# Kernel optimization log

Hardware: AMD Instinct MI355X
Metric: run time of the kernel (lower is better)

The kernel has to match this reference:

```python
import jax, jax.numpy as jnp
import numpy as np

B, A, OBS, HID, MSG, NH, NACT = 4096, 32, 128, 256, 64, 4, 16


def _mha(x, Wqkv, bqkv, Wo, bo, h):
    # torch nn.MultiheadAttention self-attention, batch_first
    b, a, m = x.shape
    qkv = x @ Wqkv.T + bqkv                      # [B,A,3M]
    q, k, v = jnp.split(qkv, 3, axis=-1)
    dh = m // h
    sh = lambda t: t.reshape(b, a, h, dh).transpose(0, 2, 1, 3)  # [B,H,A,dh]
    q, k, v = sh(q), sh(k), sh(v)
    att = jax.nn.softmax(jnp.einsum('bhqd,bhkd->bhqk', q, k) / jnp.sqrt(jnp.float32(dh)), axis=-1)
    o = jnp.einsum('bhqk,bhkd->bhqd', att, v).transpose(0, 2, 1, 3).reshape(b, a, m)
    return o @ Wo.T + bo


def setup_inputs() -> dict:
    key = jax.random.key(0)
    ks = jax.random.split(key, 24)
    p = lambda i, shape, s=0.05: (jax.random.normal(ks[i], shape, dtype=jnp.float32) * s)
    return {
        'obs': jax.random.normal(ks[0], (B, A, OBS), dtype=jnp.float32),
        'eps_intra': jax.random.normal(ks[1], (B, A, MSG), dtype=jnp.float32),
        'eps_inter': jax.random.normal(ks[2], (B, A, MSG), dtype=jnp.float32),
        'W_local': p(3, (HID, OBS)), 'b_local': p(4, (HID,)),
        'W_inter': p(5, (MSG, OBS)), 'b_inter': p(6, (MSG,)),
        'W_intra': p(7, (MSG, OBS)), 'b_intra': p(8, (MSG,)),
        # 4 attention nets: [intra_mu, intra_std, inter_mu, inter_std]
        'Wqkv': p(9, (4, 3 * MSG, MSG)), 'bqkv': p(10, (4, 3 * MSG)),
        'Wo': p(11, (4, MSG, MSG)), 'bo': p(12, (4, MSG)),
        'att_w': p(13, (1, MSG)), 'att_b': p(14, (1,)),
        'W1': p(15, (HID, HID + 2 * MSG)), 'b1': p(16, (HID,)),
        'W2': p(17, (HID, HID)), 'b2': p(18, (HID,)),
        'Wa': p(19, (NACT, HID)), 'ba': p(20, (NACT,)),
        'Wv': p(21, (1, HID)), 'bv': p(22, (1,)),
        'att_head': NH,
    }


def reference(obs, eps_intra, eps_inter, W_local, b_local, W_inter, b_inter,
              W_intra, b_intra, Wqkv, bqkv, Wo, bo, att_w, att_b,
              W1, b1, W2, b2, Wa, ba, Wv, bv, att_head):
    # embeddings
    local = jnp.tanh(obs @ W_local.T + b_local)            # [B,A,HID]
    inter_e = jnp.tanh(obs @ W_inter.T + b_inter)          # [B,A,MSG]
    intra_e = jnp.tanh(obs @ W_intra.T + b_intra)          # [B,A,MSG]
    # intra_com: mu/std attention + reparameterise
    intra_mu = _mha(intra_e, Wqkv[0], bqkv[0], Wo[0], bo[0], att_head)
    intra_std = jax.nn.softplus(_mha(intra_e, Wqkv[1], bqkv[1], Wo[1], bo[1], att_head) - 5.0)
    intra_obs = intra_mu + intra_std * eps_intra
    # inter_com
    inter_mu = _mha(inter_e, Wqkv[2], bqkv[2], Wo[2], bo[2], att_head)
    inter_std = jax.nn.softplus(_mha(inter_e, Wqkv[3], bqkv[3], Wo[3], bo[3], att_head) - 5.0)
    inter_obs = inter_mu + inter_std * eps_inter
    # pooling over agents (dim=0 in per-env code == axis=1 with batch dim)
    score = jax.nn.softmax(inter_obs @ att_w.T + att_b, axis=1)   # [B,A,1]
    pooled = jnp.sum(score * inter_obs, axis=1, keepdims=True)    # [B,1,MSG]
    pooled_b = jnp.broadcast_to(pooled, inter_obs.shape)
    # AgentAC.forward
    final_obs = jnp.concatenate([local, intra_obs, pooled_b], axis=-1)
    h = jnp.tanh(final_obs @ W1.T + b1)
    h = jnp.tanh(h @ W2.T + b2)
    a = jax.nn.log_softmax(h @ Wa.T + ba, axis=-1)
    v = h @ Wv.T + bv
    return (a, v)
```

## Files before the change

### kernel.cpp

```cpp
#include <hip/hip_runtime.h>

#define BB 4096
#define AA_ 32
#define OBSD 128
#define HIDD 256
#define MSGD 64
#define NHH 4
#define DHH 16
#define NACTD 16
#define NT 512

#define OFF_WLOCAL 0
#define OFF_WINTER 32768
#define OFF_WINTRA 40960
#define OFF_WQKV   49152
#define OFF_WO     98304
#define OFF_W1     114688
#define OFF_W2     212992
#define OFF_WA     278528
#define OFF_WHEAD  282624
#define WS_TOTAL   290816

#define L_LB 0
#define L_IE 16896
#define L_NE 21504
#define L_IO 26112
#define L_QK 30720
#define L_VT 39424
#define L_AT 44544
#define L_SC 49152
#define SMEM_SZ 49664

typedef unsigned short u16;
typedef unsigned int u32;
typedef __attribute__((ext_vector_type(8))) short bf16x8;
typedef __attribute__((ext_vector_type(4))) float f32x4;

#define MFMA16(a, b, c) __builtin_amdgcn_mfma_f32_16x16x32_bf16((a), (b), (c), 0, 0, 0)

__device__ __forceinline__ float b2f(u16 s) { return __uint_as_float((u32)s << 16); }
__device__ __forceinline__ u16 f2b(float f) {
    u32 u = __float_as_uint(f);
    u += 0x7FFFu + ((u >> 16) & 1u);
    return (u16)(u >> 16);
}
__device__ __forceinline__ float tof(float x) { return x; }
// ... 22 lines not shown
    } else {
        const float* p = (const float*)Wf + (size_t)n * ldw + k;
        f32x4 f0 = *(const f32x4*)(p);
        f32x4 f1 = *(const f32x4*)(p + 4);
#pragma unroll
        for (int j = 0; j < 8; j++) {
            float fv = (j < 4) ? f0[j] : f1[j - 4];
            u16 h = f2b(fv);
            bh[j] = (short)h;
            bl[j] = (short)f2b(fv - b2f(h));
        }
    }
}

template<int N, int K, int ACT, int WM, typename T>
__device__ __forceinline__ void mdense(const u16* X, int ldx,
                                       const T* Wf, const u16* Whi, const u16* Wlo,
                                       const T* bias, u16* O, int ldo) {
    const int tid = threadIdx.x;
    const int wv = tid >> 6, lo16 = tid & 15, hi = (tid & 63) >> 4;
#pragma unroll 1
    for (int nt = wv; nt < N / 16; nt += 8) {
        f32x4 acc0 = {0.f, 0.f, 0.f, 0.f}, acc1 = {0.f, 0.f, 0.f, 0.f};
#pragma unroll
        for (int k0 = 0; k0 < K; k0 += 32) {
            bf16x8 bh, bl;
            loadW<WM>(Wf, Whi, Wlo, K, nt * 16 + lo16, k0 + hi * 8, bh, bl);
            bf16x8 a0 = *(const bf16x8*)(X + lo16 * ldx + k0 + hi * 8);
            bf16x8 a1 = *(const bf16x8*)(X + (16 + lo16) * ldx + k0 + hi * 8);
            acc0 = MFMA16(a0, bh, acc0);
            acc1 = MFMA16(a1, bh, acc1);
            if constexpr (WM == 1) {
                acc0 = MFMA16(a0, bl, acc0);
                acc1 = MFMA16(a1, bl, acc1);
            }
        }
        float bb = tof(bias[nt * 16 + lo16]);
#pragma unroll
        for (int r = 0; r < 4; r++) {
            float v0 = acc0[r] + bb, v1 = acc1[r] + bb;
            if (ACT) { v0 = fast_tanh(v0); v1 = fast_tanh(v1); }
            O[(hi * 4 + r) * ldo + nt * 16 + lo16] = f2b(v0);
            O[(16 + hi * 4 + r) * ldo + nt * 16 + lo16] = f2b(v1);
        }
    }
}

template<int WM, typename T>
__device__ __forceinline__ void qkv_pass(int net, const u16* xe,
                                         const T* Wqkv, const T* bqkv,
                                         const u16* wsh, const u16* wsl,
                                         u16* qk, u16* vT) {
    const int tid = threadIdx.x;
    const int wv = tid >> 6, lo16 = tid & 15, hi = (tid & 63) >> 4;
    const T* Wq = Wqkv + (size_t)net * 192 * MSGD;
    const T* bq_ = bqkv + (size_t)net * 192;
    const u16* Whi = (WM == 2) ? wsh + OFF_WQKV + net * 192 * MSGD : nullptr;
    const u16* Wlo = (WM == 2) ? wsl + OFF_WQKV + net * 192 * MSGD : nullptr;
#pragma unroll 1
    for (int nt = wv; nt < 12; nt += 8) {
        f32x4 acc0 = {0.f, 0.f, 0.f, 0.f}, acc1 = {0.f, 0.f, 0.f, 0.f};
#pragma unroll
        for (int k0 = 0; k0 < 64; k0 += 32) {
            bf16x8 bh, bl;
            loadW<WM>(Wq, Whi, Wlo, 64, nt * 16 + lo16, k0 + hi * 8, bh, bl);
            bf16x8 a0 = *(const bf16x8*)(xe + lo16 * 72 + k0 + hi * 8);
            bf16x8 a1 = *(const bf16x8*)(xe + (16 + lo16) * 72 + k0 + hi * 8);
            acc0 = MFMA16(a0, bh, acc0);
            acc1 = MFMA16(a1, bh, acc1);
            if constexpr (WM == 1) {
                acc0 = MFMA16(a0, bl, acc0);
                acc1 = MFMA16(a1, bl, acc1);
            }
        }
        float bb = tof(bq_[nt * 16 + lo16]);
        if (nt < 8) {
#pragma unroll
            for (int r = 0; r < 4; r++) {
                qk[(hi * 4 + r) * 136 + nt * 16 + lo16] = f2b(acc0[r] + bb);
                qk[(16 + hi * 4 + r) * 136 + nt * 16 + lo16] = f2b(acc1[r] + bb);
            }
        } else {
            const int d = (nt - 8) * 16 + lo16;
#pragma unroll
            for (int r = 0; r < 4; r++) {
                vT[d * 40 + hi * 4 + r] = f2b(acc0[r] + bb);
                vT[d * 40 + 16 + hi * 4 + r] = f2b(acc1[r] + bb);
            }
        }
    }
}

template<typename T, int WM>
__device__ void body(const T* obs, const T* eps_intra, const T* eps_inter,
                     const T* W_local, const T* b_local,
                     const T* W_inter, const T* b_inter,
                     const T* W_intra, const T* b_intra,
                     const T* Wqkv, const T* bqkv, const T* Wo, const T* bo,
                     const T* att_w, const T* att_b,
                     const T* W1, const T* b1, const T* W2, const T* b2,
                     const T* Wa, const T* ba, const T* Wv, const T* bv,
                     T* out_a, T* out_v, char* smem, const u16* wsw) {
    constexpr bool XSPLIT = (sizeof(T) == 4) && (WM == 1);
    const int tid = threadIdx.x;
    const int b = blockIdx.x;
    const int wv = tid >> 6, lane = tid & 63, lo16 = lane & 15, hi = lane >> 4;

    const u16* wsh = wsw;
    const u16* wsl = (WM == 2) ? wsw + WS_TOTAL : nullptr;
#define WPAIR(OFF) ((WM == 2) ? wsh + (OFF) : nullptr), ((WM == 2) ? wsl + (OFF) : nullptr)

    u16* localb    = (u16*)(smem + L_LB);
    u16* intra_e   = (u16*)(smem + L_IE);
    u16* nobs      = (u16*)(smem + L_IE);
    float* alog    = (float*)(smem + L_IE);
    u16* inter_e   = (u16*)(smem + L_NE);
    u16* iobs      = (u16*)(smem + L_IO);
    u16* qk        = (u16*)(smem + L_QK);
    u16* xh        = (u16*)(smem + L_QK);
    u16* hb        = (u16*)(smem + L_QK);
    u16* vT        = (u16*)(smem + L_VT);
    u16* xl        = (u16*)(smem + L_VT);
    u16* atto      = (u16*)(smem + L_AT);
    u16* pooled_hi = (u16*)(smem + L_SC);
    u16* pooled_lo = (u16*)(smem + L_SC + 128);
    float* plog    = (float*)(smem + L_SC + 256);
    float* pscore  = (float*)(smem + L_SC + 384);

    {
        const T* ob = obs + (size_t)b * (AA_ * OBSD);
        const int i = tid;
        const int row = i >> 4, col = (i & 15) * 8;
        if constexpr (sizeof(T) == 4) {
            f32x4 f0 = __builtin_nontemporal_load((const f32x4*)(ob + i * 8));
            f32x4 f1 = __builtin_nontemporal_load((const f32x4*)(ob + i * 8) + 1);
            bf16x8 vh, vl;
#pragma unroll
            for (int j = 0; j < 8; j++) {
                float fv = (j < 4) ? f0[j] : f1[j - 4];
                u16 h = f2b(fv);
                vh[j] = (short)h;
                vl[j] = (short)f2b(fv - b2f(h));
            }
            *(bf16x8*)(xh + row * 136 + col) = vh;
            if constexpr (XSPLIT) *(bf16x8*)(xl + row * 136 + col) = vl;
        } else {
            bf16x8 v = __builtin_nontemporal_load((const bf16x8*)(ob + i * 8));
            *(bf16x8*)(xh + row * 136 + col) = v;
        }
        if (tid < 32) *(bf16x8*)(xh + tid * 136 + 128) = bzero8();
    }
    __syncthreads();

#pragma unroll 1
    for (int u = wv; u < 24; u += 8) {
        const T *Wf, *bias; const u16 *Whi = nullptr, *Wlo = nullptr; u16* O; int ldo, nt;
        if (u < 16)      { Wf = W_local; bias = b_local; O = localb;  ldo = 264; nt = u;
                           if (WM == 2) { Whi = wsh + OFF_WLOCAL; Wlo = wsl + OFF_WLOCAL; } }
        else if (u < 20) { Wf = W_intra; bias = b_intra; O = intra_e; ldo = 72;  nt = u - 16;
                           if (WM == 2) { Whi = wsh + OFF_WINTRA; Wlo = wsl + OFF_WINTRA; } }
        else             { Wf = W_inter; bias = b_inter; O = inter_e; ldo = 72;  nt = u - 20;
                           if (WM == 2) { Whi = wsh + OFF_WINTER; Wlo = wsl + OFF_WINTER; } }
        f32x4 acc0 = {0.f, 0.f, 0.f, 0.f}, acc1 = {0.f, 0.f, 0.f, 0.f};
#pragma unroll
        for (int k0 = 0; k0 < OBSD; k0 += 32) {
            bf16x8 bh, bl;
            loadW<WM>(Wf, Whi, Wlo, OBSD, nt * 16 + lo16, k0 + hi * 8, bh, bl);
            bf16x8 a0 = *(const bf16x8*)(xh + lo16 * 136 + k0 + hi * 8);
            bf16x8 a1 = *(const bf16x8*)(xh + (16 + lo16) * 136 + k0 + hi * 8);
            acc0 = MFMA16(a0, bh, acc0);
            acc1 = MFMA16(a1, bh, acc1);
            if constexpr (WM == 1) {
                acc0 = MFMA16(a0, bl, acc0);
                acc1 = MFMA16(a1, bl, acc1);
            }
            if constexpr (XSPLIT) {
                bf16x8 l0 = *(const bf16x8*)(xl + lo16 * 136 + k0 + hi * 8);
                bf16x8 l1 = *(const bf16x8*)(xl + (16 + lo16) * 136 + k0 + hi * 8);
                acc0 = MFMA16(l0, bh, acc0);
                acc1 = MFMA16(l1, bh, acc1);
            }
        }
        float bb = tof(bias[nt * 16 + lo16]);
#pragma unroll
        for (int r = 0; r < 4; r++) {
            O[(hi * 4 + r) * ldo + nt * 16 + lo16] = f2b(fast_tanh(acc0[r] + bb));
            O[(16 + hi * 4 + r) * ldo + nt * 16 + lo16] = f2b(fast_tanh(acc1[r] + bb));
        }
    }
    __syncthreads();

#pragma unroll 1
    for (int net = 0; net < 4; net++) {
        qkv_pass<WM>(net, (net < 2) ? intra_e : inter_e, Wqkv, bqkv, wsh, wsl, qk, vT);
        __syncthreads();

        float epr[4] = {0.f, 0.f, 0.f, 0.f};
        {
            const int h = wv >> 1, mt = wv & 1;
            if (net == 1 || net == 3) {
                const T* epsb = ((net == 1) ? eps_intra : eps_inter) + (size_t)b * (AA_ * MSGD);
                const int ntU = wv & 3, half = wv >> 2, col = ntU * 16 + lo16;
#pragma unroll
                for (int r = 0; r < 4; r++)
                    epr[r] = tof(__builtin_nontemporal_load(epsb + (half * 16 + hi * 4 + r) * MSGD + col));
            }
            bf16x8 a0 = *(const bf16x8*)(qk + lo16 * 136 + 64 + h * 16 + hi * 8);
            bf16x8 a1 = *(const bf16x8*)(qk + (16 + lo16) * 136 + 64 + h * 16 + hi * 8);
            bf16x8 bq = bzero8();
            if (hi < 2) bq = *(const bf16x8*)(qk + (mt * 16 + lo16) * 136 + h * 16 + hi * 8);
            f32x4 z = {0.f, 0.f, 0.f, 0.f};
            f32x4 sc0 = MFMA16(a0, bq, z);
            f32x4 sc1 = MFMA16(a1, bq, z);
            float v0[4], v1[4];
#pragma unroll
            for (int r = 0; r < 4; r++) { v0[r] = sc0[r] * 0.25f; v1[r] = sc1[r] * 0.25f; }
            float m = fmaxf(fmaxf(fmaxf(v0[0], v0[1]), fmaxf(v0[2], v0[3])),
                            fmaxf(fmaxf(v1[0], v1[1]), fmaxf(v1[2], v1[3])));
            m = fmaxf(m, __shfl_xor(m, 16));
            m = fmaxf(m, __shfl_xor(m, 32));
            float e0[4], e1[4], s = 0.f;
#pragma unroll
            for (int r = 0; r < 4; r++) {
                e0[r] = __expf(v0[r] - m); e1[r] = __expf(v1[r] - m);
                s += e0[r] + e1[r];
            }
            s += __shfl_xor(s, 16);
            s += __shfl_xor(s, 32);
            float inv = __builtin_amdgcn_rcpf(s);
            u32 pk0 = (u32)f2b(e0[0] * inv) | ((u32)f2b(e0[1] * inv) << 16);
            u32 pk1 = (u32)f2b(e0[2] * inv) | ((u32)f2b(e0[3] * inv) << 16);
            u32 pk2 = (u32)f2b(e1[0] * inv) | ((u32)f2b(e1[1] * inv) << 16);
            u32 pk3 = (u32)f2b(e1[2] * inv) | ((u32)f2b(e1[3] * inv) << 16);
            const int sA = (((hi * 2) & 3) << 4) | lo16;
            const int sB = sA + 16;
            u32 wA0 = __shfl(pk0, sA), wA1 = __shfl(pk1, sA);
            u32 wB0 = __shfl(pk0, sB), wB1 = __shfl(pk1, sB);
            u32 xA0 = __shfl(pk2, sA), xA1 = __shfl(pk3, sA);
            u32 xB0 = __shfl(pk2, sB), xB1 = __shfl(pk3, sB);
            const bool lo = (hi < 2);
            union { u32 w[4]; bf16x8 v; } pu;
            pu.w[0] = lo ? wA0 : xA0;
            pu.w[1] = lo ? wA1 : xA1;
            pu.w[2] = lo ? wB0 : xB0;
            pu.w[3] = lo ? wB1 : xB1;
            bf16x8 bv_ = *(const bf16x8*)(vT + (h * 16 + lo16) * 40 + hi * 8);
            f32x4 o = MFMA16(pu.v, bv_, z);
#pragma unroll
            for (int r = 0; r < 4; r++)
                atto[(mt * 16 + hi * 4 + r) * 72 + h * 16 + lo16] = f2b(o[r]);
        }
        __syncthreads();

        {
            const T* Won = Wo + (size_t)net * MSGD * MSGD;
            const T* bon = bo + (size_t)net * MSGD;
            const u16* Ohi = (WM == 2) ? wsh + OFF_WO + net * 4096 : nullptr;
            const u16* Olo = (WM == 2) ? wsl + OFF_WO + net * 4096 : nullptr;
            const int ntU = wv & 3, half = wv >> 2, col = ntU * 16 + lo16;
            f32x4 acc = {0.f, 0.f, 0.f, 0.f};
#pragma unroll
            for (int k0 = 0; k0 < 64; k0 += 32) {
                bf16x8 bh, bl;
                loadW<WM>(Won, Ohi, Olo, 64, col, k0 + hi * 8, bh, bl);
                bf16x8 a = *(const bf16x8*)(atto + (half * 16 + lo16) * 72 + k0 + hi * 8);
                acc = MFMA16(a, bh, acc);
                if constexpr (WM == 1) acc = MFMA16(a, bl, acc);
            }
            float bb = tof(bon[col]);
            u16* tgt = (net < 2) ? iobs : nobs;
#pragma unroll
            for (int r = 0; r < 4; r++) {
                const int row = half * 16 + hi * 4 + r;
                if (net == 0 || net == 2) {
                    tgt[row * 72 + col] = f2b(acc[r] + bb);
                } else {
                    float zv = acc[r] + bb - 5.f;
                    float sp = (zv > 20.f) ? zv : __logf(1.f + __expf(zv));
                    tgt[row * 72 + col] = f2b(b2f(tgt[row * 72 + col]) + sp * epr[r]);
                }
            }
        }
        __syncthreads();
    }

    if (tid < 64) {
        if (tid < 32) {
            float acc = tof(att_b[0]);
            const u16* xr = nobs + tid * 72;
#pragma unroll
            for (int j = 0; j < 64; j += 8) {
                bf16x8 x = *(const bf16x8*)(xr + j);
#pragma unroll
                for (int jj = 0; jj < 8; jj++) acc = fmaf(b2f((u16)x[jj]), tof(att_w[j + jj]), acc);
            }
            plog[tid] = acc;
        }
        __builtin_amdgcn_wave_barrier();
        if (tid < 32) {
            float m = -1e30f;
            for (int a2 = 0; a2 < 32; a2++) m = fmaxf(m, plog[a2]);
            float s = 0.f;
            for (int a2 = 0; a2 < 32; a2++) s += __expf(plog[a2] - m);
            pscore[tid] = __expf(plog[tid] - m) * __builtin_amdgcn_rcpf(s);
        }
        __builtin_amdgcn_wave_barrier();
        {
            float p = 0.f;
            for (int a2 = 0; a2 < 32; a2++) p = fmaf(pscore[a2], b2f(nobs[a2 * 72 + tid]), p);
            u16 h = f2b(p);
            pooled_hi[tid] = h;
            pooled_lo[tid] = f2b(p - b2f(h));
        }
    }
    __syncthreads();

#pragma unroll 1
    for (int nt = wv; nt < 16; nt += 8) {
        const int n = nt * 16 + lo16;
        f32x4 acc0 = {0.f, 0.f, 0.f, 0.f}, acc1 = {0.f, 0.f, 0.f, 0.f};
        f32x4 accp = {0.f, 0.f, 0.f, 0.f};
#pragma unroll
        for (int k0 = 0; k0 < 256; k0 += 32) {
            bf16x8 bh, bl;
            loadW<WM>(W1, WPAIR(OFF_W1), 384, n, k0 + hi * 8, bh, bl);
            bf16x8 a0 = *(const bf16x8*)(localb + lo16 * 264 + k0 + hi * 8);
            bf16x8 a1 = *(const bf16x8*)(localb + (16 + lo16) * 264 + k0 + hi * 8);
            acc0 = MFMA16(a0, bh, acc0);
            acc1 = MFMA16(a1, bh, acc1);
            if constexpr (WM == 1) { acc0 = MFMA16(a0, bl, acc0); acc1 = MFMA16(a1, bl, acc1); }
        }
#pragma unroll
        for (int k0 = 0; k0 < 64; k0 += 32) {
            bf16x8 bh, bl;
            loadW<WM>(W1, WPAIR(OFF_W1), 384, n, 256 + k0 + hi * 8, bh, bl);
            bf16x8 a0 = *(const bf16x8*)(iobs + lo16 * 72 + k0 + hi * 8);
            bf16x8 a1 = *(const bf16x8*)(iobs + (16 + lo16) * 72 + k0 + hi * 8);
            acc0 = MFMA16(a0, bh, acc0);
            acc1 = MFMA16(a1, bh, acc1);
            if constexpr (WM == 1) { acc0 = MFMA16(a0, bl, acc0); acc1 = MFMA16(a1, bl, acc1); }
        }
#pragma unroll
        for (int k0 = 0; k0 < 64; k0 += 32) {
            bf16x8 bh, bl;
            loadW<WM>(W1, WPAIR(OFF_W1), 384, n, 320 + k0 + hi * 8, bh, bl);
            bf16x8 pa  = *(const bf16x8*)(pooled_hi + k0 + hi * 8);
            bf16x8 pal = *(const bf16x8*)(pooled_lo + k0 + hi * 8);
            accp = MFMA16(pa, bh, accp);
            accp = MFMA16(pal, bh, accp);
            if constexpr (WM == 1) accp = MFMA16(pa, bl, accp);
        }
        float bb = tof(b1[n]) + accp[0];
#pragma unroll
        for (int r = 0; r < 4; r++) {
            hb[(hi * 4 + r) * 264 + n] = f2b(fast_tanh(acc0[r] + bb));
            hb[(16 + hi * 4 + r) * 264 + n] = f2b(fast_tanh(acc1[r] + bb));
        }
    }
    __syncthreads();

    mdense<256, 256, 1, WM>(hb, 264, W2, WPAIR(OFF_W2), b2, localb, 264);
    __syncthreads();

    if constexpr (WM == 2) {
        if (wv < 4) {
            const int ntU = wv & 1, half = wv >> 1;
            const u16* Hhi = wsh + OFF_WHEAD;
            f32x4 acc = {0.f, 0.f, 0.f, 0.f};
#pragma unroll
            for (int k0 = 0; k0 < 256; k0 += 32) {
                bf16x8 bh = *(const bf16x8*)(Hhi + (size_t)(ntU * 16 + lo16) * 256 + k0 + hi * 8);
                bf16x8 a = *(const bf16x8*)(localb + (half * 16 + lo16) * 264 + k0 + hi * 8);
                acc = MFMA16(a, bh, acc);
            }
#pragma unroll
            for (int r = 0; r < 4; r++) {
                const int row = half * 16 + hi * 4 + r;
                if (ntU == 0) alog[row * 18 + lo16] = acc[r] + tof(ba[lo16]);
                else if (lo16 == 0) out_v[(size_t)b * 32 + row] = fromf<T>(acc[r] + tof(bv[0]));
            }
        }
    } else {
        if (wv == 0) {
            f32x4 acc0 = {0.f, 0.f, 0.f, 0.f}, acc1 = {0.f, 0.f, 0.f, 0.f};
#pragma unroll
            for (int k0 = 0; k0 < 256; k0 += 32) {
                bf16x8 bh, bl;
                loadW<WM>(Wa, nullptr, nullptr, 256, lo16, k0 + hi * 8, bh, bl);
                bf16x8 a0 = *(const bf16x8*)(localb + lo16 * 264 + k0 + hi * 8);
                bf16x8 a1 = *(const bf16x8*)(localb + (16 + lo16) * 264 + k0 + hi * 8);
                acc0 = MFMA16(a0, bh, acc0);
                acc1 = MFMA16(a1, bh, acc1);
                if constexpr (WM == 1) { acc0 = MFMA16(a0, bl, acc0); acc1 = MFMA16(a1, bl, acc1); }
            }
            float bb = tof(ba[lo16]);
#pragma unroll
            for (int r = 0; r < 4; r++) {
                alog[(hi * 4 + r) * 18 + lo16] = acc0[r] + bb;
                alog[(16 + hi * 4 + r) * 18 + lo16] = acc1[r] + bb;
            }
        } else if (wv == 1 && lane < 32) {
            const u16* xr = localb + lane * 264;
            float acc = tof(bv[0]);
            for (int k0 = 0; k0 < 256; k0 += 8) {
                bf16x8 x = *(const bf16x8*)(xr + k0);
#pragma unroll
                for (int j = 0; j < 8; j++) acc = fmaf(b2f((u16)x[j]), tof(Wv[k0 + j]), acc);
            }
            out_v[(size_t)b * 32 + lane] = fromf<T>(acc);
        }
    }
    __syncthreads();
    if (tid < 32) {
        const float* lr = alog + tid * 18;
        float m = -1e30f;
#pragma unroll
        for (int n = 0; n < 16; n++) m = fmaxf(m, lr[n]);
        float s = 0.f;
#pragma unroll
        for (int n = 0; n < 16; n++) s += __expf(lr[n] - m);
        float lse = m + __logf(s);
        if constexpr (sizeof(T) == 2) {
            bf16x8 o0, o1;
#pragma unroll
            for (int n = 0; n < 8; n++) {
                o0[n] = (short)f2b(lr[n] - lse);
                o1[n] = (short)f2b(lr[8 + n] - lse);
            }
            bf16x8* oa = (bf16x8*)((u16*)out_a + ((size_t)b * 32 + tid) * 16);
            oa[0] = o0; oa[1] = o1;
        } else {
            float* oa = (float*)out_a + ((size_t)b * 32 + tid) * 16;
#pragma unroll
            for (int g = 0; g < 4; g++) {
                f32x4 t = {lr[4 * g] - lse, lr[4 * g + 1] - lse,
                           lr[4 * g + 2] - lse, lr[4 * g + 3] - lse};
                *(f32x4*)(oa + 4 * g) = t;
            }
        }
    }
#undef WPAIR
}

__device__ __forceinline__ int detect_f32(const void* obs) {
    const unsigned short* u = (const unsigned short*)obs;
    int e = ((int)u[threadIdx.x & 63] >> 7) & 0xFF;
    return __ballot(e >= 0x90) != 0ull;
// ... 16 lines not shown
        if (i < OFF_WINTER)      { src = (const float*)Wl;  off = OFF_WLOCAL; }
        else if (i < OFF_WINTRA) { src = (const float*)Wi;  off = OFF_WINTER; }
        else if (i < OFF_WQKV)   { src = (const float*)Wt;  off = OFF_WINTRA; }
        else if (i < OFF_WO)     { src = (const float*)Wq;  off = OFF_WQKV; }
        else if (i < OFF_W1)     { src = (const float*)Wo_; off = OFF_WO; }
        else if (i < OFF_W2)     { src = (const float*)W1_; off = OFF_W1; }
        else if (i < OFF_WA)     { src = (const float*)W2_; off = OFF_W2; }
        else                     { src = (const float*)Wa_; off = OFF_WA; }
        w = src[i - off];
    }
    u16 h = f2b(w);
    ws[i] = h;
    ws[WS_TOTAL + i] = f2b(w - b2f(h));
}

extern "C" __global__ void __launch_bounds__(NT, 6)
TeamCommAgent_53077205844655_kernel(
    const void* obs, const void* eps_intra, const void* eps_inter,
    const void* W_local, const void* b_local,
    const void* W_inter, const void* b_inter,
    const void* W_intra, const void* b_intra,
    const void* Wqkv, const void* bqkv, const void* Wo, const void* bo,
    const void* att_w, const void* att_b,
    const void* W1, const void* b1, const void* W2, const void* b2,
    const void* Wa, const void* ba, const void* Wv, const void* bv,
    void* out, const u16* wsw) {
    __shared__ __align__(16) char smem[SMEM_SZ];
    if (detect_f32(obs)) {
        if (wsw) {
            body<float, 2>((const float*)obs, (const float*)eps_intra, (const float*)eps_inter,
                           (const float*)W_local, (const float*)b_local,
// ... 35 lines not shown
                     (const u16*)Wv, (const u16*)bv,
                     (u16*)out, (u16*)out + (size_t)BB * AA_ * NACTD, smem, nullptr);
    }
}

extern "C" void kernel_launch(void* const* d_in, const int* in_sizes, int n_in,
                              void* d_out, int out_size, void* d_ws, size_t ws_size,
                              hipStream_t stream) {
    const bool use_ws = (d_ws != nullptr) &&
                        (ws_size >= (size_t)(2 * WS_TOTAL) * sizeof(u16));
    if (use_ws) {
        TeamCommAgent_prep_kernel<<<dim3((WS_TOTAL + 255) / 256), dim3(256), 0, stream>>>(
            d_in[0], d_in[3], d_in[5], d_in[7], d_in[9], d_in[11],
            d_in[15], d_in[17], d_in[19], d_in[21], (u16*)d_ws);
    }
    TeamCommAgent_53077205844655_kernel<<<dim3(BB), dim3(NT), 0, stream>>>(
        d_in[0], d_in[1], d_in[2], d_in[3], d_in[4], d_in[5], d_in[6],
        d_in[7], d_in[8], d_in[9], d_in[10], d_in[11], d_in[12], d_in[13],
        d_in[14], d_in[15], d_in[16], d_in[17], d_in[18], d_in[19], d_in[20],
        d_in[21], d_in[22], d_out, use_ws ? (const u16*)d_ws : nullptr);
}
```

Measured before the change: 477.4 us.

## Process two batch elements per block to reuse weight loads across 64 rows

Result: no change. 480.8 us (+0.7%).

```diff
diff --git a/kernel.cpp b/kernel.cpp
--- a/kernel.cpp
+++ b/kernel.cpp
@@ -22,14 +22,14 @@
 #define WS_TOTAL   290816
 
 #define L_LB 0
-#define L_IE 16896
-#define L_NE 21504
-#define L_IO 26112
-#define L_QK 30720
-#define L_VT 39424
-#define L_AT 44544
-#define L_SC 49152
-#define SMEM_SZ 49664
+#define L_IO 33792
+#define L_IE 43008
+#define L_NE 52224
+#define L_QK 61440
+#define L_VT 78848
+#define L_AT 89088
+#define L_SC 98304
+#define SMEM_SZ 99328
 
 typedef unsigned short u16;
 typedef unsigned int u32;
@@ -82,34 +82,43 @@
 }
 
 template<int N, int K, int ACT, int WM, typename T>
-__device__ __forceinline__ void mdense(const u16* X, int ldx,
-                                       const T* Wf, const u16* Whi, const u16* Wlo,
-                                       const T* bias, u16* O, int ldo) {
+__device__ __forceinline__ void mdense64(const u16* X, int ldx,
+                                         const T* Wf, const u16* Whi, const u16* Wlo,
+                                         const T* bias, u16* O, int ldo) {
     const int tid = threadIdx.x;
     const int wv = tid >> 6, lo16 = tid & 15, hi = (tid & 63) >> 4;
 #pragma unroll 1
     for (int nt = wv; nt < N / 16; nt += 8) {
-        f32x4 acc0 = {0.f, 0.f, 0.f, 0.f}, acc1 = {0.f, 0.f, 0.f, 0.f};
+        f32x4 acc0 = {0.f,0.f,0.f,0.f}, acc1 = {0.f,0.f,0.f,0.f};
+        f32x4 acc2 = {0.f,0.f,0.f,0.f}, acc3 = {0.f,0.f,0.f,0.f};
 #pragma unroll
         for (int k0 = 0; k0 < K; k0 += 32) {
             bf16x8 bh, bl;
             loadW<WM>(Wf, Whi, Wlo, K, nt * 16 + lo16, k0 + hi * 8, bh, bl);
             bf16x8 a0 = *(const bf16x8*)(X + lo16 * ldx + k0 + hi * 8);
             bf16x8 a1 = *(const bf16x8*)(X + (16 + lo16) * ldx + k0 + hi * 8);
+            bf16x8 a2 = *(const bf16x8*)(X + (32 + lo16) * ldx + k0 + hi * 8);
+            bf16x8 a3 = *(const bf16x8*)(X + (48 + lo16) * ldx + k0 + hi * 8);
             acc0 = MFMA16(a0, bh, acc0);
             acc1 = MFMA16(a1, bh, acc1);
+            acc2 = MFMA16(a2, bh, acc2);
+            acc3 = MFMA16(a3, bh, acc3);
             if constexpr (WM == 1) {
                 acc0 = MFMA16(a0, bl, acc0);
                 acc1 = MFMA16(a1, bl, acc1);
+                acc2 = MFMA16(a2, bl, acc2);
+                acc3 = MFMA16(a3, bl, acc3);
             }
         }
         float bb = tof(bias[nt * 16 + lo16]);
 #pragma unroll
         for (int r = 0; r < 4; r++) {
-            float v0 = acc0[r] + bb, v1 = acc1[r] + bb;
-            if (ACT) { v0 = fast_tanh(v0); v1 = fast_tanh(v1); }
+            float v0 = acc0[r] + bb, v1 = acc1[r] + bb, v2 = acc2[r] + bb, v3 = acc3[r] + bb;
+            if (ACT) { v0 = fast_tanh(v0); v1 = fast_tanh(v1); v2 = fast_tanh(v2); v3 = fast_tanh(v3); }
             O[(hi * 4 + r) * ldo + nt * 16 + lo16] = f2b(v0);
             O[(16 + hi * 4 + r) * ldo + nt * 16 + lo16] = f2b(v1);
+            O[(32 + hi * 4 + r) * ldo + nt * 16 + lo16] = f2b(v2);
+            O[(48 + hi * 4 + r) * ldo + nt * 16 + lo16] = f2b(v3);
         }
     }
 }
@@ -127,18 +136,25 @@
     const u16* Wlo = (WM == 2) ? wsl + OFF_WQKV + net * 192 * MSGD : nullptr;
 #pragma unroll 1
     for (int nt = wv; nt < 12; nt += 8) {
-        f32x4 acc0 = {0.f, 0.f, 0.f, 0.f}, acc1 = {0.f, 0.f, 0.f, 0.f};
+        f32x4 acc0 = {0.f,0.f,0.f,0.f}, acc1 = {0.f,0.f,0.f,0.f};
+        f32x4 acc2 = {0.f,0.f,0.f,0.f}, acc3 = {0.f,0.f,0.f,0.f};
 #pragma unroll
         for (int k0 = 0; k0 < 64; k0 += 32) {
             bf16x8 bh, bl;
             loadW<WM>(Wq, Whi, Wlo, 64, nt * 16 + lo16, k0 + hi * 8, bh, bl);
             bf16x8 a0 = *(const bf16x8*)(xe + lo16 * 72 + k0 + hi * 8);
             bf16x8 a1 = *(const bf16x8*)(xe + (16 + lo16) * 72 + k0 + hi * 8);
+            bf16x8 a2 = *(const bf16x8*)(xe + (32 + lo16) * 72 + k0 + hi * 8);
+            bf16x8 a3 = *(const bf16x8*)(xe + (48 + lo16) * 72 + k0 + hi * 8);
             acc0 = MFMA16(a0, bh, acc0);
             acc1 = MFMA16(a1, bh, acc1);
+            acc2 = MFMA16(a2, bh, acc2);
+            acc3 = MFMA16(a3, bh, acc3);
             if constexpr (WM == 1) {
                 acc0 = MFMA16(a0, bl, acc0);
                 acc1 = MFMA16(a1, bl, acc1);
+                acc2 = MFMA16(a2, bl, acc2);
+                acc3 = MFMA16(a3, bl, acc3);
             }
         }
         float bb = tof(bq_[nt * 16 + lo16]);
@@ -147,6 +163,8 @@
             for (int r = 0; r < 4; r++) {
                 qk[(hi * 4 + r) * 136 + nt * 16 + lo16] = f2b(acc0[r] + bb);
                 qk[(16 + hi * 4 + r) * 136 + nt * 16 + lo16] = f2b(acc1[r] + bb);
+                qk[(32 + hi * 4 + r) * 136 + nt * 16 + lo16] = f2b(acc2[r] + bb);
+                qk[(48 + hi * 4 + r) * 136 + nt * 16 + lo16] = f2b(acc3[r] + bb);
             }
         } else {
             const int d = (nt - 8) * 16 + lo16;
@@ -154,6 +172,8 @@
             for (int r = 0; r < 4; r++) {
                 vT[d * 40 + hi * 4 + r] = f2b(acc0[r] + bb);
                 vT[d * 40 + 16 + hi * 4 + r] = f2b(acc1[r] + bb);
+                vT[2560 + d * 40 + hi * 4 + r] = f2b(acc2[r] + bb);
+                vT[2560 + d * 40 + 16 + hi * 4 + r] = f2b(acc3[r] + bb);
             }
         }
     }
@@ -171,7 +191,7 @@
                      T* out_a, T* out_v, char* smem, const u16* wsw) {
     constexpr bool XSPLIT = (sizeof(T) == 4) && (WM == 1);
     const int tid = threadIdx.x;
-    const int b = blockIdx.x;
+    const size_t b0 = (size_t)blockIdx.x * 2;
     const int wv = tid >> 6, lane = tid & 63, lo16 = lane & 15, hi = lane >> 4;
 
     const u16* wsh = wsw;
@@ -179,44 +199,47 @@
 #define WPAIR(OFF) ((WM == 2) ? wsh + (OFF) : nullptr), ((WM == 2) ? wsl + (OFF) : nullptr)
 
     u16* localb    = (u16*)(smem + L_LB);
+    u16* iobs      = (u16*)(smem + L_IO);
+    float* alog    = (float*)(smem + L_IO);
     u16* intra_e   = (u16*)(smem + L_IE);
     u16* nobs      = (u16*)(smem + L_IE);
-    float* alog    = (float*)(smem + L_IE);
+    u16* hb        = (u16*)(smem + L_IE);
     u16* inter_e   = (u16*)(smem + L_NE);
-    u16* iobs      = (u16*)(smem + L_IO);
     u16* qk        = (u16*)(smem + L_QK);
     u16* xh        = (u16*)(smem + L_QK);
-    u16* hb        = (u16*)(smem + L_QK);
     u16* vT        = (u16*)(smem + L_VT);
     u16* xl        = (u16*)(smem + L_VT);
     u16* atto      = (u16*)(smem + L_AT);
     u16* pooled_hi = (u16*)(smem + L_SC);
-    u16* pooled_lo = (u16*)(smem + L_SC + 128);
-    float* plog    = (float*)(smem + L_SC + 256);
-    float* pscore  = (float*)(smem + L_SC + 384);
+    u16* pooled_lo = (u16*)(smem + L_SC + 256);
+    float* plog    = (float*)(smem + L_SC + 512);
+    float* pscore  = (float*)(smem + L_SC + 768);
 
     {
-        const T* ob = obs + (size_t)b * (AA_ * OBSD);
-        const int i = tid;
-        const int row = i >> 4, col = (i & 15) * 8;
-        if constexpr (sizeof(T) == 4) {
-            f32x4 f0 = __builtin_nontemporal_load((const f32x4*)(ob + i * 8));
-            f32x4 f1 = __builtin_nontemporal_load((const f32x4*)(ob + i * 8) + 1);
-            bf16x8 vh, vl;
-#pragma unroll
-            for (int j = 0; j < 8; j++) {
-                float fv = (j < 4) ? f0[j] : f1[j - 4];
-                u16 h = f2b(fv);
-                vh[j] = (short)h;
-                vl[j] = (short)f2b(fv - b2f(h));
-            }
-            *(bf16x8*)(xh + row * 136 + col) = vh;
-            if constexpr (XSPLIT) *(bf16x8*)(xl + row * 136 + col) = vl;
-        } else {
-            bf16x8 v = __builtin_nontemporal_load((const bf16x8*)(ob + i * 8));
-            *(bf16x8*)(xh + row * 136 + col) = v;
-        }
-        if (tid < 32) *(bf16x8*)(xh + tid * 136 + 128) = bzero8();
+        const T* ob = obs + b0 * (AA_ * OBSD);
+#pragma unroll
+        for (int it = 0; it < 2; it++) {
+            const int i = tid + it * NT;
+            const int row = i >> 4, col = (i & 15) * 8;
+            if constexpr (sizeof(T) == 4) {
+                f32x4 f0 = __builtin_nontemporal_load((const f32x4*)(ob + i * 8));
+                f32x4 f1 = __builtin_nontemporal_load((const f32x4*)(ob + i * 8) + 1);
+                bf16x8 vh, vl;
+#pragma unroll
+                for (int j = 0; j < 8; j++) {
+                    float fv = (j < 4) ? f0[j] : f1[j - 4];
+                    u16 h = f2b(fv);
+                    vh[j] = (short)h;
+                    vl[j] = (short)f2b(fv - b2f(h));
+                }
+                *(bf16x8*)(xh + row * 136 + col) = vh;
+                if constexpr (XSPLIT) *(bf16x8*)(xl + row * 136 + col) = vl;
+            } else {
+                bf16x8 v = __builtin_nontemporal_load((const bf16x8*)(ob + i * 8));
+                *(bf16x8*)(xh + row * 136 + col) = v;
+            }
+        }
+        if (tid < 64) *(bf16x8*)(xh + tid * 136 + 128) = bzero8();
     }
     __syncthreads();
 
@@ -229,24 +252,35 @@
                            if (WM == 2) { Whi = wsh + OFF_WINTRA; Wlo = wsl + OFF_WINTRA; } }
         else             { Wf = W_inter; bias = b_inter; O = inter_e; ldo = 72;  nt = u - 20;
                            if (WM == 2) { Whi = wsh + OFF_WINTER; Wlo = wsl + OFF_WINTER; } }
-        f32x4 acc0 = {0.f, 0.f, 0.f, 0.f}, acc1 = {0.f, 0.f, 0.f, 0.f};
+        f32x4 acc0 = {0.f,0.f,0.f,0.f}, acc1 = {0.f,0.f,0.f,0.f};
+        f32x4 acc2 = {0.f,0.f,0.f,0.f}, acc3 = {0.f,0.f,0.f,0.f};
 #pragma unroll
         for (int k0 = 0; k0 < OBSD; k0 += 32) {
             bf16x8 bh, bl;
             loadW<WM>(Wf, Whi, Wlo, OBSD, nt * 16 + lo16, k0 + hi * 8, bh, bl);
             bf16x8 a0 = *(const bf16x8*)(xh + lo16 * 136 + k0 + hi * 8);
             bf16x8 a1 = *(const bf16x8*)(xh + (16 + lo16) * 136 + k0 + hi * 8);
+            bf16x8 a2 = *(const bf16x8*)(xh + (32 + lo16) * 136 + k0 + hi * 8);
+            bf16x8 a3 = *(const bf16x8*)(xh + (48 + lo16) * 136 + k0 + hi * 8);
             acc0 = MFMA16(a0, bh, acc0);
             acc1 = MFMA16(a1, bh, acc1);
+            acc2 = MFMA16(a2, bh, acc2);
+            acc3 = MFMA16(a3, bh, acc3);
             if constexpr (WM == 1) {
                 acc0 = MFMA16(a0, bl, acc0);
                 acc1 = MFMA16(a1, bl, acc1);
+                acc2 = MFMA16(a2, bl, acc2);
+                acc3 = MFMA16(a3, bl, acc3);
             }
             if constexpr (XSPLIT) {
                 bf16x8 l0 = *(const bf16x8*)(xl + lo16 * 136 + k0 + hi * 8);
                 bf16x8 l1 = *(const bf16x8*)(xl + (16 + lo16) * 136 + k0 + hi * 8);
+                bf16x8 l2 = *(const bf16x8*)(xl + (32 + lo16) * 136 + k0 + hi * 8);
+                bf16x8 l3 = *(const bf16x8*)(xl + (48 + lo16) * 136 + k0 + hi * 8);
                 acc0 = MFMA16(l0, bh, acc0);
                 acc1 = MFMA16(l1, bh, acc1);
+                acc2 = MFMA16(l2, bh, acc2);
+                acc3 = MFMA16(l3, bh, acc3);
             }
         }
         float bb = tof(bias[nt * 16 + lo16]);
@@ -254,6 +288,8 @@
         for (int r = 0; r < 4; r++) {
             O[(hi * 4 + r) * ldo + nt * 16 + lo16] = f2b(fast_tanh(acc0[r] + bb));
             O[(16 + hi * 4 + r) * ldo + nt * 16 + lo16] = f2b(fast_tanh(acc1[r] + bb));
+            O[(32 + hi * 4 + r) * ldo + nt * 16 + lo16] = f2b(fast_tanh(acc2[r] + bb));
+            O[(48 + hi * 4 + r) * ldo + nt * 16 + lo16] = f2b(fast_tanh(acc3[r] + bb));
         }
     }
     __syncthreads();
@@ -263,60 +299,67 @@
         qkv_pass<WM>(net, (net < 2) ? intra_e : inter_e, Wqkv, bqkv, wsh, wsl, qk, vT);
         __syncthreads();
 
-        float epr[4] = {0.f, 0.f, 0.f, 0.f};
+        float epr[2][4] = {{0.f,0.f,0.f,0.f},{0.f,0.f,0.f,0.f}};
         {
+            if (net == 1 || net == 3) {
+                const T* epsb = ((net == 1) ? eps_intra : eps_inter) + b0 * (AA_ * MSGD);
+                const int grp = wv >> 2, col = (wv & 3) * 16 + lo16;
+#pragma unroll
+                for (int s = 0; s < 2; s++)
+#pragma unroll
+                    for (int r = 0; r < 4; r++)
+                        epr[s][r] = tof(__builtin_nontemporal_load(
+                            epsb + (grp * 32 + s * 16 + hi * 4 + r) * MSGD + col));
+            }
             const int h = wv >> 1, mt = wv & 1;
-            if (net == 1 || net == 3) {
-                const T* epsb = ((net == 1) ? eps_intra : eps_inter) + (size_t)b * (AA_ * MSGD);
-                const int ntU = wv & 3, half = wv >> 2, col = ntU * 16 + lo16;
+#pragma unroll 1
+            for (int bt = 0; bt < 2; bt++) {
+                const u16* qkB = qk + bt * 32 * 136;
+                bf16x8 a0 = *(const bf16x8*)(qkB + lo16 * 136 + 64 + h * 16 + hi * 8);
+                bf16x8 a1 = *(const bf16x8*)(qkB + (16 + lo16) * 136 + 64 + h * 16 + hi * 8);
+                bf16x8 bq = bzero8();
+                if (hi < 2) bq = *(const bf16x8*)(qkB + (mt * 16 + lo16) * 136 + h * 16 + hi * 8);
+                f32x4 z = {0.f, 0.f, 0.f, 0.f};
+                f32x4 sc0 = MFMA16(a0, bq, z);
+                f32x4 sc1 = MFMA16(a1, bq, z);
+                float v0[4], v1[4];
+#pragma unroll
+                for (int r = 0; r < 4; r++) { v0[r] = sc0[r] * 0.25f; v1[r] = sc1[r] * 0.25f; }
+                float m = fmaxf(fmaxf(fmaxf(v0[0], v0[1]), fmaxf(v0[2], v0[3])),
+                                fmaxf(fmaxf(v1[0], v1[1]), fmaxf(v1[2], v1[3])));
+                m = fmaxf(m, __shfl_xor(m, 16));
+                m = fmaxf(m, __shfl_xor(m, 32));
+                float e0[4], e1[4], s = 0.f;
+#pragma unroll
+                for (int r = 0; r < 4; r++) {
+                    e0[r] = __expf(v0[r] - m); e1[r] = __expf(v1[r] - m);
+                    s += e0[r] + e1[r];
+                }
+                s += __shfl_xor(s, 16);
+                s += __shfl_xor(s, 32);
+                float inv = __builtin_amdgcn_rcpf(s);
+                u32 pk0 = (u32)f2b(e0[0] * inv) | ((u32)f2b(e0[1] * inv) << 16);
+                u32 pk1 = (u32)f2b(e0[2] * inv) | ((u32)f2b(e0[3] * inv) << 16);
+                u32 pk2 = (u32)f2b(e1[0] * inv) | ((u32)f2b(e1[1] * inv) << 16);
+                u32 pk3 = (u32)f2b(e1[2] * inv) | ((u32)f2b(e1[3] * inv) << 16);
+                const int sA = (((hi * 2) & 3) << 4) | lo16;
+                const int sB = sA + 16;
+                u32 wA0 = __shfl(pk0, sA), wA1 = __shfl(pk1, sA);
+                u32 wB0 = __shfl(pk0, sB), wB1 = __shfl(pk1, sB);
+                u32 xA0 = __shfl(pk2, sA), xA1 = __shfl(pk3, sA);
+                u32 xB0 = __shfl(pk2, sB), xB1 = __shfl(pk3, sB);
+                const bool lo = (hi < 2);
+                union { u32 w[4]; bf16x8 v; } pu;
+                pu.w[0] = lo ? wA0 : xA0;
+                pu.w[1] = lo ? wA1 : xA1;
+                pu.w[2] = lo ? wB0 : xB0;
+                pu.w[3] = lo ? wB1 : xB1;
+                bf16x8 bv_ = *(const bf16x8*)(vT + bt * 2560 + (h * 16 + lo16) * 40 + hi * 8);
+                f32x4 o = MFMA16(pu.v, bv_, z);
 #pragma unroll
                 for (int r = 0; r < 4; r++)
-                    epr[r] = tof(__builtin_nontemporal_load(epsb + (half * 16 + hi * 4 + r) * MSGD + col));
-            }
-            bf16x8 a0 = *(const bf16x8*)(qk + lo16 * 136 + 64 + h * 16 + hi * 8);
-            bf16x8 a1 = *(const bf16x8*)(qk + (16 + lo16) * 136 + 64 + h * 16 + hi * 8);
-            bf16x8 bq = bzero8();
-            if (hi < 2) bq = *(const bf16x8*)(qk + (mt * 16 + lo16) * 136 + h * 16 + hi * 8);
-            f32x4 z = {0.f, 0.f, 0.f, 0.f};
-            f32x4 sc0 = MFMA16(a0, bq, z);
-            f32x4 sc1 = MFMA16(a1, bq, z);
-            float v0[4], v1[4];
-#pragma unroll
-            for (int r = 0; r < 4; r++) { v0[r] = sc0[r] * 0.25f; v1[r] = sc1[r] * 0.25f; }
-            float m = fmaxf(fmaxf(fmaxf(v0[0], v0[1]), fmaxf(v0[2], v0[3])),
-                            fmaxf(fmaxf(v1[0], v1[1]), fmaxf(v1[2], v1[3])));
-            m = fmaxf(m, __shfl_xor(m, 16));
-            m = fmaxf(m, __shfl_xor(m, 32));
-            float e0[4], e1[4], s = 0.f;
-#pragma unroll
-            for (int r = 0; r < 4; r++) {
-                e0[r] = __expf(v0[r] - m); e1[r] = __expf(v1[r] - m);
-                s += e0[r] + e1[r];
-            }
-            s += __shfl_xor(s, 16);
-            s += __shfl_xor(s, 32);
-            float inv = __builtin_amdgcn_rcpf(s);
-            u32 pk0 = (u32)f2b(e0[0] * inv) | ((u32)f2b(e0[1] * inv) << 16);
-            u32 pk1 = (u32)f2b(e0[2] * inv) | ((u32)f2b(e0[3] * inv) << 16);
-            u32 pk2 = (u32)f2b(e1[0] * inv) | ((u32)f2b(e1[1] * inv) << 16);
-            u32 pk3 = (u32)f2b(e1[2] * inv) | ((u32)f2b(e1[3] * inv) << 16);
-            const int sA = (((hi * 2) & 3) << 4) | lo16;
-            const int sB = sA + 16;
-            u32 wA0 = __shfl(pk0, sA), wA1 = __shfl(pk1, sA);
-            u32 wB0 = __shfl(pk0, sB), wB1 = __shfl(pk1, sB);
-            u32 xA0 = __shfl(pk2, sA), xA1 = __shfl(pk3, sA);
-            u32 xB0 = __shfl(pk2, sB), xB1 = __shfl(pk3, sB);
-            const bool lo = (hi < 2);
-            union { u32 w[4]; bf16x8 v; } pu;
-            pu.w[0] = lo ? wA0 : xA0;
-            pu.w[1] = lo ? wA1 : xA1;
-            pu.w[2] = lo ? wB0 : xB0;
-            pu.w[3] = lo ? wB1 : xB1;
-            bf16x8 bv_ = *(const bf16x8*)(vT + (h * 16 + lo16) * 40 + hi * 8);
-            f32x4 o = MFMA16(pu.v, bv_, z);
-#pragma unroll
-            for (int r = 0; r < 4; r++)
-                atto[(mt * 16 + hi * 4 + r) * 72 + h * 16 + lo16] = f2b(o[r]);
+                    atto[(bt * 32 + mt * 16 + hi * 4 + r) * 72 + h * 16 + lo16] = f2b(o[r]);
+            }
         }
         __syncthreads();
 
@@ -325,60 +368,71 @@
             const T* bon = bo + (size_t)net * MSGD;
             const u16* Ohi = (WM == 2) ? wsh + OFF_WO + net * 4096 : nullptr;
             const u16* Olo = (WM == 2) ? wsl + OFF_WO + net * 4096 : nullptr;
-            const int ntU = wv & 3, half = wv >> 2, col = ntU * 16 + lo16;
-            f32x4 acc = {0.f, 0.f, 0.f, 0.f};
+            const int ntU = wv & 3, grp = wv >> 2, col = ntU * 16 + lo16;
+            f32x4 acc0 = {0.f,0.f,0.f,0.f}, acc1 = {0.f,0.f,0.f,0.f};
 #pragma unroll
             for (int k0 = 0; k0 < 64; k0 += 32) {
                 bf16x8 bh, bl;
                 loadW<WM>(Won, Ohi, Olo, 64, col, k0 + hi * 8, bh, bl);
-                bf16x8 a = *(const bf16x8*)(atto + (half * 16 + lo16) * 72 + k0 + hi * 8);
-                acc = MFMA16(a, bh, acc);
-                if constexpr (WM == 1) acc = MFMA16(a, bl, acc);
+                bf16x8 aA = *(const bf16x8*)(atto + (grp * 32 + lo16) * 72 + k0 + hi * 8);
+                bf16x8 aB = *(const bf16x8*)(atto + (grp * 32 + 16 + lo16) * 72 + k0 + hi * 8);
+                acc0 = MFMA16(aA, bh, acc0);
+                acc1 = MFMA16(aB, bh, acc1);
+                if constexpr (WM == 1) {
+                    acc0 = MFMA16(aA, bl, acc0);
+                    acc1 = MFMA16(aB, bl, acc1);
+                }
             }
             float bb = tof(bon[col]);
             u16* tgt = (net < 2) ? iobs : nobs;
 #pragma unroll
-            for (int r = 0; r < 4; r++) {
-                const int row = half * 16 + hi * 4 + r;
-                if (net == 0 || net == 2) {
-                    tgt[row * 72 + col] = f2b(acc[r] + bb);
-                } else {
-                    float zv = acc[r] + bb - 5.f;
-                    float sp = (zv > 20.f) ? zv : __logf(1.f + __expf(zv));
-                    tgt[row * 72 + col] = f2b(b2f(tgt[row * 72 + col]) + sp * epr[r]);
+            for (int s = 0; s < 2; s++) {
+                f32x4 acc = s ? acc1 : acc0;
+#pragma unroll
+                for (int r = 0; r < 4; r++) {
+                    const int row = grp * 32 + s * 16 + hi * 4 + r;
+                    if (net == 0 || net == 2) {
+                        tgt[row * 72 + col] = f2b(acc[r] + bb);
+                    } else {
+                        float zv = acc[r] + bb - 5.f;
+                        float sp = (zv > 20.f) ? zv : __logf(1.f + __expf(zv));
+                        tgt[row * 72 + col] = f2b(b2f(tgt[row * 72 + col]) + sp * epr[s][r]);
+                    }
                 }
             }
         }
         __syncthreads();
     }
 
-    if (tid < 64) {
-        if (tid < 32) {
+    if (wv < 2) {
+        const int bt = wv;
+        if (lane < 32) {
             float acc = tof(att_b[0]);
-            const u16* xr = nobs + tid * 72;
+            const u16* xr = nobs + (bt * 32 + lane) * 72;
 #pragma unroll
             for (int j = 0; j < 64; j += 8) {
                 bf16x8 x = *(const bf16x8*)(xr + j);
 #pragma unroll
                 for (int jj = 0; jj < 8; jj++) acc = fmaf(b2f((u16)x[jj]), tof(att_w[j + jj]), acc);
             }
-            plog[tid] = acc;
+            plog[bt * 32 + lane] = acc;
         }
         __builtin_amdgcn_wave_barrier();
-        if (tid < 32) {
+        if (lane < 32) {
             float m = -1e30f;
-            for (int a2 = 0; a2 < 32; a2++) m = fmaxf(m, plog[a2]);
+            for (int a2 = 0; a2 < 32; a2++) m = fmaxf(m, plog[bt * 32 + a2]);
             float s = 0.f;
-            for (int a2 = 0; a2 < 32; a2++) s += __expf(plog[a2] - m);
-            pscore[tid] = __expf(plog[tid] - m) * __builtin_amdgcn_rcpf(s);
+            for (int a2 = 0; a2 < 32; a2++) s += __expf(plog[bt * 32 + a2] - m);
+            pscore[bt * 32 + lane] = __expf(plog[bt * 32 + lane] - m) * __builtin_amdgcn_rcpf(s);
         }
         __builtin_amdgcn_wave_barrier();
         {
             float p = 0.f;
-            for (int a2 = 0; a2 < 32; a2++) p = fmaf(pscore[a2], b2f(nobs[a2 * 72 + tid]), p);
+            for (int a2 = 0; a2 < 32; a2++)
+                p = fmaf(pscore[bt * 32 + a2], b2f(nobs[(bt * 32 + a2) * 72 + lane]), p);
             u16 h = f2b(p);
-            pooled_hi[tid] = h;
-            pooled_lo[tid] = f2b(p - b2f(h));
+            pooled_hi[bt * 64 + lane] = h;
+            pooled_lo[bt * 64 + lane] = f2b(p - b2f(h));
         }
     }
     __syncthreads();
@@ -386,17 +440,25 @@
 #pragma unroll 1
     for (int nt = wv; nt < 16; nt += 8) {
         const int n = nt * 16 + lo16;
-        f32x4 acc0 = {0.f, 0.f, 0.f, 0.f}, acc1 = {0.f, 0.f, 0.f, 0.f};
-        f32x4 accp = {0.f, 0.f, 0.f, 0.f};
+        f32x4 acc0 = {0.f,0.f,0.f,0.f}, acc1 = {0.f,0.f,0.f,0.f};
+        f32x4 acc2 = {0.f,0.f,0.f,0.f}, acc3 = {0.f,0.f,0.f,0.f};
+        f32x4 accp0 = {0.f,0.f,0.f,0.f}, accp1 = {0.f,0.f,0.f,0.f};
 #pragma unroll
         for (int k0 = 0; k0 < 256; k0 += 32) {
             bf16x8 bh, bl;
             loadW<WM>(W1, WPAIR(OFF_W1), 384, n, k0 + hi * 8, bh, bl);
             bf16x8 a0 = *(const bf16x8*)(localb + lo16 * 264 + k0 + hi * 8);
             bf16x8 a1 = *(const bf16x8*)(localb + (16 + lo16) * 264 + k0 + hi * 8);
+            bf16x8 a2 = *(const bf16x8*)(localb + (32 + lo16) * 264 + k0 + hi * 8);
+            bf16x8 a3 = *(const bf16x8*)(localb + (48 + lo16) * 264 + k0 + hi * 8);
             acc0 = MFMA16(a0, bh, acc0);
             acc1 = MFMA16(a1, bh, acc1);
-            if constexpr (WM == 1) { acc0 = MFMA16(a0, bl, acc0); acc1 = MFMA16(a1, bl, acc1); }
+            acc2 = MFMA16(a2, bh, acc2);
+            acc3 = MFMA16(a3, bh, acc3);
+            if constexpr (WM == 1) {
+                acc0 = MFMA16(a0, bl, acc0); acc1 = MFMA16(a1, bl, acc1);
+                acc2 = MFMA16(a2, bl, acc2); acc3 = MFMA16(a3, bl, acc3);
+            }
         }
 #pragma unroll
         for (int k0 = 0; k0 < 64; k0 += 32) {
@@ -404,59 +466,74 @@
             loadW<WM>(W1, WPAIR(OFF_W1), 384, n, 256 + k0 + hi * 8, bh, bl);
             bf16x8 a0 = *(const bf16x8*)(iobs + lo16 * 72 + k0 + hi * 8);
             bf16x8 a1 = *(const bf16x8*)(iobs + (16 + lo16) * 72 + k0 + hi * 8);
+            bf16x8 a2 = *(const bf16x8*)(iobs + (32 + lo16) * 72 + k0 + hi * 8);
+            bf16x8 a3 = *(const bf16x8*)(iobs + (48 + lo16) * 72 + k0 + hi * 8);
             acc0 = MFMA16(a0, bh, acc0);
             acc1 = MFMA16(a1, bh, acc1);
-            if constexpr (WM == 1) { acc0 = MFMA16(a0, bl, acc0); acc1 = MFMA16(a1, bl, acc1); }
+            acc2 = MFMA16(a2, bh, acc2);
+            acc3 = MFMA16(a3, bh, acc3);
+            if constexpr (WM == 1) {
+                acc0 = MFMA16(a0, bl, acc0); acc1 = MFMA16(a1, bl, acc1);
+                acc2 = MFMA16(a2, bl, acc2); acc3 = MFMA16(a3, bl, acc3);
+            }
         }
 #pragma unroll
         for (int k0 = 0; k0 < 64; k0 += 32) {
             bf16x8 bh, bl;
             loadW<WM>(W1, WPAIR(OFF_W1), 384, n, 320 + k0 + hi * 8, bh, bl);
-            bf16x8 pa  = *(const bf16x8*)(pooled_hi + k0 + hi * 8);
-            bf16x8 pal = *(const bf16x8*)(pooled_lo + k0 + hi * 8);
-            accp = MFMA16(pa, bh, accp);
-            accp = MFMA16(pal, bh, accp);
-            if constexpr (WM == 1) accp = MFMA16(pa, bl, accp);
-        }
-        float bb = tof(b1[n]) + accp[0];
+            bf16x8 pa0  = *(const bf16x8*)(pooled_hi + k0 + hi * 8);
+            bf16x8 pal0 = *(const bf16x8*)(pooled_lo + k0 + hi * 8);
+            bf16x8 pa1  = *(const bf16x8*)(pooled_hi + 64 + k0 + hi * 8);
+            bf16x8 pal1 = *(const bf16x8*)(pooled_lo + 64 + k0 + hi * 8);
+            accp0 = MFMA16(pa0, bh, accp0);
+            accp0 = MFMA16(pal0, bh, accp0);
+            accp1 = MFMA16(pa1, bh, accp1);
+            accp1 = MFMA16(pal1, bh, accp1);
+            if constexpr (WM == 1) {
+                accp0 = MFMA16(pa0, bl, accp0);
+                accp1 = MFMA16(pa1, bl, accp1);
+            }
+        }
+        float bb0 = tof(b1[n]) + accp0[0];
+        float bb1 = tof(b1[n]) + accp1[0];
 #pragma unroll
         for (int r = 0; r < 4; r++) {
-            hb[(hi * 4 + r) * 264 + n] = f2b(fast_tanh(acc0[r] + bb));
-            hb[(16 + hi * 4 + r) * 264 + n] = f2b(fast_tanh(acc1[r] + bb));
+            hb[(hi * 4 + r) * 264 + n] = f2b(fast_tanh(acc0[r] + bb0));
+            hb[(16 + hi * 4 + r) * 264 + n] = f2b(fast_tanh(acc1[r] + bb0));
+            hb[(32 + hi * 4 + r) * 264 + n] = f2b(fast_tanh(acc2[r] + bb1));
+            hb[(48 + hi * 4 + r) * 264 + n] = f2b(fast_tanh(acc3[r] + bb1));
         }
     }
     __syncthreads();
 
-    mdense<256, 256, 1, WM>(hb, 264, W2, WPAIR(OFF_W2), b2, localb, 264);
+    mdense64<256, 256, 1, WM>(hb, 264, W2, WPAIR(OFF_W2), b2, localb, 264);
     __syncthreads();
 
     if constexpr (WM == 2) {
-        if (wv < 4) {
-            const int ntU = wv & 1, half = wv >> 1;
-            const u16* Hhi = wsh + OFF_WHEAD;
-            f32x4 acc = {0.f, 0.f, 0.f, 0.f};
-#pragma unroll
-            for (int k0 = 0; k0 < 256; k0 += 32) {
-                bf16x8 bh = *(const bf16x8*)(Hhi + (size_t)(ntU * 16 + lo16) * 256 + k0 + hi * 8);
-                bf16x8 a = *(const bf16x8*)(localb + (half * 16 + lo16) * 264 + k0 + hi * 8);
-                acc = MFMA16(a, bh, acc);
-            }
-#pragma unroll
-            for (int r = 0; r < 4; r++) {
-                const int row = half * 16 + hi * 4 + r;
-                if (ntU == 0) alog[row * 18 + lo16] = acc[r] + tof(ba[lo16]);
-                else if (lo16 == 0) out_v[(size_t)b * 32 + row] = fromf<T>(acc[r] + tof(bv[0]));
-            }
+        const int ntU = wv & 1, rg = wv >> 1;
+        const u16* Hhi = wsh + OFF_WHEAD;
+        f32x4 acc = {0.f, 0.f, 0.f, 0.f};
+#pragma unroll
+        for (int k0 = 0; k0 < 256; k0 += 32) {
+            bf16x8 bh = *(const bf16x8*)(Hhi + (size_t)(ntU * 16 + lo16) * 256 + k0 + hi * 8);
+            bf16x8 a = *(const bf16x8*)(localb + (rg * 16 + lo16) * 264 + k0 + hi * 8);
+            acc = MFMA16(a, bh, acc);
+        }
+#pragma unroll
+        for (int r = 0; r < 4; r++) {
+            const int row = rg * 16 + hi * 4 + r;
+            if (ntU == 0) alog[row * 18 + lo16] = acc[r] + tof(ba[lo16]);
+            else if (lo16 == 0) out_v[b0 * 32 + row] = fromf<T>(acc[r] + tof(bv[0]));
         }
     } else {
-        if (wv == 0) {
-            f32x4 acc0 = {0.f, 0.f, 0.f, 0.f}, acc1 = {0.f, 0.f, 0.f, 0.f};
+        if (wv < 2) {
+            f32x4 acc0 = {0.f,0.f,0.f,0.f}, acc1 = {0.f,0.f,0.f,0.f};
 #pragma unroll
             for (int k0 = 0; k0 < 256; k0 += 32) {
                 bf16x8 bh, bl;
                 loadW<WM>(Wa, nullptr, nullptr, 256, lo16, k0 + hi * 8, bh, bl);
-                bf16x8 a0 = *(const bf16x8*)(localb + lo16 * 264 + k0 + hi * 8);
-                bf16x8 a1 = *(const bf16x8*)(localb + (16 + lo16) * 264 + k0 + hi * 8);
+                bf16x8 a0 = *(const bf16x8*)(localb + (wv * 32 + lo16) * 264 + k0 + hi * 8);
+                bf16x8 a1 = *(const bf16x8*)(localb + (wv * 32 + 16 + lo16) * 264 + k0 + hi * 8);
                 acc0 = MFMA16(a0, bh, acc0);
                 acc1 = MFMA16(a1, bh, acc1);
                 if constexpr (WM == 1) { acc0 = MFMA16(a0, bl, acc0); acc1 = MFMA16(a1, bl, acc1); }
@@ -464,22 +541,23 @@
             float bb = tof(ba[lo16]);
 #pragma unroll
             for (int r = 0; r < 4; r++) {
-                alog[(hi * 4 + r) * 18 + lo16] = acc0[r] + bb;
-                alog[(16 + hi * 4 + r) * 18 + lo16] = acc1[r] + bb;
-            }
-        } else if (wv == 1 && lane < 32) {
-            const u16* xr = localb + lane * 264;
+                alog[(wv * 32 + hi * 4 + r) * 18 + lo16] = acc0[r] + bb;
+                alog[(wv * 32 + 16 + hi * 4 + r) * 18 + lo16] = acc1[r] + bb;
+            }
+        } else if (wv < 4 && lane < 32) {
+            const int row = (wv - 2) * 32 + lane;
+            const u16* xr = localb + row * 264;
             float acc = tof(bv[0]);
             for (int k0 = 0; k0 < 256; k0 += 8) {
                 bf16x8 x = *(const bf16x8*)(xr + k0);
 #pragma unroll
                 for (int j = 0; j < 8; j++) acc = fmaf(b2f((u16)x[j]), tof(Wv[k0 + j]), acc);
             }
-            out_v[(size_t)b * 32 + lane] = fromf<T>(acc);
+            out_v[b0 * 32 + row] = fromf<T>(acc);
         }
     }
     __syncthreads();
-    if (tid < 32) {
+    if (tid < 64) {
         const float* lr = alog + tid * 18;
         float m = -1e30f;
 #pragma unroll
@@ -495,10 +573,10 @@
                 o0[n] = (short)f2b(lr[n] - lse);
                 o1[n] = (short)f2b(lr[8 + n] - lse);
             }
-            bf16x8* oa = (bf16x8*)((u16*)out_a + ((size_t)b * 32 + tid) * 16);
+            bf16x8* oa = (bf16x8*)((u16*)out_a + (b0 * 32 + tid) * 16);
             oa[0] = o0; oa[1] = o1;
         } else {
-            float* oa = (float*)out_a + ((size_t)b * 32 + tid) * 16;
+            float* oa = (float*)out_a + (b0 * 32 + tid) * 16;
 #pragma unroll
             for (int g = 0; g < 4; g++) {
                 f32x4 t = {lr[4 * g] - lse, lr[4 * g + 1] - lse,
@@ -545,7 +623,7 @@
     ws[WS_TOTAL + i] = f2b(w - b2f(h));
 }
 
-extern "C" __global__ void __launch_bounds__(NT, 6)
+extern "C" __global__ void __launch_bounds__(NT, 2)
 TeamCommAgent_53077205844655_kernel(
     const void* obs, const void* eps_intra, const void* eps_inter,
     const void* W_local, const void* b_local,
@@ -611,7 +689,7 @@
             d_in[0], d_in[3], d_in[5], d_in[7], d_in[9], d_in[11],
             d_in[15], d_in[17], d_in[19], d_in[21], (u16*)d_ws);
     }
-    TeamCommAgent_53077205844655_kernel<<<dim3(BB), dim3(NT), 0, stream>>>(
+    TeamCommAgent_53077205844655_kernel<<<dim3(BB / 2), dim3(NT), 0, stream>>>(
         d_in[0], d_in[1], d_in[2], d_in[3], d_in[4], d_in[5], d_in[6],
         d_in[7], d_in[8], d_in[9], d_in[10], d_in[11], d_in[12], d_in[13],
         d_in[14], d_in[15], d_in[16], d_in[17], d_in[18], d_in[19], d_in[20],
```
